# Optimization experiments

Hardware: AMD Instinct MI355X
Metric: run time of the kernel (lower is better)

## Reference

```python
import jax, jax.numpy as jnp
import numpy as np

D_MODEL, N_HEADS, D_HEAD, D_MLP = 768, 12, 64, 3072
B, S = 2, 2048
EPS = 1e-5
IGNORE = -100000.0
INIT = 0.02


def gelu_new(x):
    # GPT-2 'new' gelu: 0.5*x*(1+tanh(sqrt(2/pi)*(x+0.044715*x^3)))
    c = np.sqrt(2.0 / np.pi).astype(np.float32)
    return 0.5 * x * (1.0 + jnp.tanh(c * (x + 0.044715 * x ** 3)))


def layernorm(x, w, b):
    mean = jnp.mean(x, axis=-1, keepdims=True)
    var = jnp.var(x, axis=-1, keepdims=True)
    return (x - mean) / jnp.sqrt(var + EPS) * w + b


def setup_inputs() -> dict:
    key = jax.random.key(0)
    ks = jax.random.split(key, 8)
    return {
        "resid_pre": jax.random.normal(ks[0], (B, S, D_MODEL), dtype=jnp.float32),
        "W_Q": INIT * jax.random.normal(ks[1], (N_HEADS, D_MODEL, D_HEAD), dtype=jnp.float32),
        "b_Q": jnp.zeros((N_HEADS, D_HEAD), jnp.float32),
        "W_K": INIT * jax.random.normal(ks[2], (N_HEADS, D_MODEL, D_HEAD), dtype=jnp.float32),
        "b_K": jnp.zeros((N_HEADS, D_HEAD), jnp.float32),
        "W_V": INIT * jax.random.normal(ks[3], (N_HEADS, D_MODEL, D_HEAD), dtype=jnp.float32),
        "b_V": jnp.zeros((N_HEADS, D_HEAD), jnp.float32),
        "W_O": INIT * jax.random.normal(ks[4], (N_HEADS, D_HEAD, D_MODEL), dtype=jnp.float32),
        "b_O": jnp.zeros((D_MODEL,), jnp.float32),
        "ln1_w": jnp.ones((D_MODEL,), jnp.float32),
        "ln1_b": jnp.zeros((D_MODEL,), jnp.float32),
        "ln2_w": jnp.ones((D_MODEL,), jnp.float32),
        "ln2_b": jnp.zeros((D_MODEL,), jnp.float32),
        "W_in": INIT * jax.random.normal(ks[5], (D_MODEL, D_MLP), dtype=jnp.float32),
        "b_in": jnp.zeros((D_MLP,), jnp.float32),
        "W_out": INIT * jax.random.normal(ks[6], (D_MLP, D_MODEL), dtype=jnp.float32),
        "b_out": jnp.zeros((D_MODEL,), jnp.float32),
    }


def attention(x, W_Q, b_Q, W_K, b_K, W_V, b_V, W_O, b_O):
    # x: [b, s, e]
    q = jnp.einsum('bse,neh->bsnh', x, W_Q) + b_Q
    k = jnp.einsum('bse,neh->bsnh', x, W_K) + b_K
    v = jnp.einsum('bse,neh->bsnh', x, W_V) + b_V
    scores = jnp.einsum('bknh,bqnh->bnqk', k, q) / np.float32(np.sqrt(D_HEAD))
    s = x.shape[1]
    mask = jnp.tril(jnp.ones((s, s), jnp.float32))  # [sq, sk]
    scores = mask * scores + (1.0 - mask) * IGNORE
    probs = jax.nn.softmax(scores, axis=-1)
    z = jnp.einsum('bnqk,bknh->bqnh', probs, v)
    out = jnp.einsum('bqnh,nhe->bqe', z, W_O) + b_O
    return out


def mlp(x, W_in, b_in, W_out, b_out):
    hidden = jnp.einsum('bse,eh->bsh', x, W_in) + b_in
    return jnp.einsum('bsh,he->bse', gelu_new(hidden), W_out) + b_out


def reference(resid_pre, W_Q, b_Q, W_K, b_K, W_V, b_V, W_O, b_O,
              ln1_w, ln1_b, ln2_w, ln2_b, W_in, b_in, W_out, b_out):
    resid_mid = attention(layernorm(resid_pre, ln1_w, ln1_b),
                          W_Q, b_Q, W_K, b_K, W_V, b_V, W_O, b_O) + resid_pre
    out = mlp(layernorm(resid_mid, ln2_w, ln2_b), W_in, b_in, W_out, b_out) + resid_mid
    return out
```

## Files before the change

kernel.cpp:

```cpp
#include <hip/hip_runtime.h>
#include <math.h>

typedef unsigned short ushort_t;
typedef __attribute__((ext_vector_type(8))) short bf16x8;
typedef __attribute__((ext_vector_type(4))) float f32x4;

#define D_MODEL 768
#define N_HEADS 12
#define D_HEAD  64
#define D_MLP   3072
#define BATCH   2
#define SEQ     2048
#define ROWS    (BATCH * SEQ)
#define LN_EPS  1e-5f
#define QKV_LD  2304

__device__ __forceinline__ ushort_t f2bf(float f) {
    unsigned u = __float_as_uint(f);
    u += 0x7fffu + ((u >> 16) & 1u);
    return (ushort_t)(u >> 16);
}
__device__ __forceinline__ float bf2f(ushort_t u) {
    return __uint_as_float((unsigned)u << 16);
}

#define GLD16(g, l) __builtin_amdgcn_global_load_lds( \
    (const __attribute__((address_space(1))) void*)(g), \
    (__attribute__((address_space(3))) void*)(l), 16, 0, 0)

__global__ __launch_bounds__(256) void ln_kernel(const float* __restrict__ x,
                                                 const float* __restrict__ w,
                                                 const float* __restrict__ b,
                                                 ushort_t* __restrict__ y) {
    int row = blockIdx.x;
    const float* xr = x + (size_t)row * D_MODEL;
    float v[3];
    float s = 0.f, sq = 0.f;
#pragma unroll
    for (int u = 0; u < 3; ++u) {
        v[u] = xr[threadIdx.x + u * 256];
        s += v[u];
        sq += v[u] * v[u];
    }
#pragma unroll
    for (int off = 32; off >= 1; off >>= 1) {
        s  += __shfl_xor(s, off);
        sq += __shfl_xor(sq, off);
    }
    __shared__ float ss[4], ssq[4];
    int wave = threadIdx.x >> 6;
    int lane = threadIdx.x & 63;
    if (lane == 0) { ss[wave] = s; ssq[wave] = sq; }
    __syncthreads();
    s = ss[0] + ss[1] + ss[2] + ss[3];
    sq = ssq[0] + ssq[1] + ssq[2] + ssq[3];
    float mean = s * (1.0f / D_MODEL);
    float var = sq * (1.0f / D_MODEL) - mean * mean;
    float rstd = rsqrtf(var + LN_EPS);
    ushort_t* yr = y + (size_t)row * D_MODEL;
#pragma unroll
    for (int u = 0; u < 3; ++u) {
        int idx = threadIdx.x + u * 256;
        yr[idx] = f2bf((v[u] - mean) * rstd * w[idx] + b[idx]);
    }
}

__device__ __forceinline__ float gelu_new_f(float x) {
    float y2 = -1.5957691216057308f * (x + 0.044715f * x * x * x);
    return x / (1.0f + __expf(y2));
}

__device__ __forceinline__ void do_transpose(const float* __restrict__ in, int in_ld, long in_zs,
                                             ushort_t* __restrict__ out, int out_ld, long out_zs,
                                             int bx, int by, int bz) {
    __shared__ float T[64][65];
    long ib = (long)bz * in_zs;
    long ob = (long)bz * out_zs;
    int r0 = bx * 64;
    int c0 = by * 64;
    int tr = threadIdx.x >> 4;
    int tc4 = (threadIdx.x & 15) * 4;
#pragma unroll
    for (int i = 0; i < 4; ++i) {
        int r = i * 16 + tr;
        float4 v = *reinterpret_cast<const float4*>(in + ib + (long)(r0 + r) * in_ld + c0 + tc4);
        T[r][tc4 + 0] = v.x; T[r][tc4 + 1] = v.y;
        T[r][tc4 + 2] = v.z; T[r][tc4 + 3] = v.w;
    }
    __syncthreads();
#pragma unroll
    for (int i = 0; i < 4; ++i) {
        int oc = i * 16 + tr;
        ushort4 o;
        o.x = f2bf(T[tc4 + 0][oc]);
        o.y = f2bf(T[tc4 + 1][oc]);
        o.z = f2bf(T[tc4 + 2][oc]);
        o.w = f2bf(T[tc4 + 3][oc]);
        *reinterpret_cast<ushort4*>(out + ob + (long)(c0 + oc) * out_ld + r0 + tc4) = o;
    }
}

__global__ __launch_bounds__(256) void prep_kernel(
        const float* __restrict__ WQ, const float* __restrict__ WK,
        const float* __restrict__ WV, const float* __restrict__ WO,
        const float* __restrict__ Win, const float* __restrict__ Wout,
        const float* __restrict__ bQ, const float* __restrict__ bK,
        const float* __restrict__ bV,
        ushort_t* __restrict__ wqkvT, ushort_t* __restrict__ woT,
        ushort_t* __restrict__ winT, ushort_t* __restrict__ woutT,
        float* __restrict__ bias_cat) {
    int id = blockIdx.x;
    if (id < 432) {
        int j = id / 144, r = id % 144;
        const float* src = (j == 0) ? WQ : (j == 1) ? WK : WV;
        do_transpose(src, 64, 49152, wqkvT + j * 589824, 768, 49152, r % 12, 0, r / 12);
    } else if (id < 576) {
        int r = id - 432;
        do_transpose(WO, 768, 0, woT, 768, 0, r % 12, r / 12, 0);
    } else if (id < 1152) {
        int r = id - 576;
        do_transpose(Win, 3072, 0, winT, 768, 0, r % 12, r / 12, 0);
    } else if (id < 1728) {
        int r = id - 1152;
        do_transpose(Wout, 768, 0, woutT, 3072, 0, r % 48, r / 48, 0);
    } else {
        for (int i = threadIdx.x; i < 768; i += 256) {
            bias_cat[i] = bQ[i];
            bias_cat[768 + i] = bK[i];
            bias_cat[1536 + i] = bV[i];
        }
    }
}

template <int MODE>
__global__ __launch_bounds__(256) void mfma_gemm(
        const ushort_t* __restrict__ A, int lda,
        const ushort_t* __restrict__ Bt, int ldb,
        const float* __restrict__ bias,
        const float* __restrict__ resid,
        void* __restrict__ C, int cld, int K) {
    __shared__ char As[16384];
    __shared__ char Bs[16384];
    int tid = threadIdx.x;
    int lane = tid & 63, wv = tid >> 6;
    int wr = wv >> 1, wc = wv & 1;
    int l15 = lane & 15, lhi = lane >> 4;
    int m0 = blockIdx.y * 128, n0 = blockIdx.x * 128;

    f32x4 acc[4][4];
#pragma unroll
    for (int i = 0; i < 4; ++i)
#pragma unroll
        for (int j = 0; j < 4; ++j) acc[i][j] = (f32x4)(0.f);

    int srow[4], scol[4];
#pragma unroll
    for (int i = 0; i < 4; ++i) {
        int p = (i * 256 + tid) << 4;
        srow[i] = p >> 7;
        scol[i] = ((p & 127) ^ ((srow[i] & 7) << 4)) >> 1;
    }
    int lbase = wv << 10;

    for (int k0 = 0; k0 < K; k0 += 64) {
#pragma unroll
        for (int i = 0; i < 4; ++i) {
            const ushort_t* ga = A + (size_t)(m0 + srow[i]) * lda + k0 + scol[i];
            GLD16(ga, As + i * 4096 + lbase);
            const ushort_t* gb = Bt + (size_t)(n0 + srow[i]) * ldb + k0 + scol[i];
            GLD16(gb, Bs + i * 4096 + lbase);
        }
        __syncthreads();

        bf16x8 af[4][2], bfr[4][2];
#pragma unroll
        for (int f = 0; f < 4; ++f)
#pragma unroll
            for (int h = 0; h < 2; ++h) {
                int ar = wr * 64 + f * 16 + l15;
                int ac = h * 64 + lhi * 16;
                af[f][h] = *reinterpret_cast<const bf16x8*>(As + ar * 128 + (ac ^ ((ar & 7) << 4)));
                int br = wc * 64 + f * 16 + l15;
                bfr[f][h] = *reinterpret_cast<const bf16x8*>(Bs + br * 128 + (ac ^ ((br & 7) << 4)));
            }
#pragma unroll
        for (int fm = 0; fm < 4; ++fm)
#pragma unroll
            for (int fn = 0; fn < 4; ++fn) {
                acc[fm][fn] = __builtin_amdgcn_mfma_f32_16x16x32_bf16(af[fm][0], bfr[fn][0], acc[fm][fn], 0, 0, 0);
                acc[fm][fn] = __builtin_amdgcn_mfma_f32_16x16x32_bf16(af[fm][1], bfr[fn][1], acc[fm][fn], 0, 0, 0);
            }
        __syncthreads();
    }

#pragma unroll
    for (int fm = 0; fm < 4; ++fm)
#pragma unroll
        for (int fn = 0; fn < 4; ++fn)
#pragma unroll
            for (int i = 0; i < 4; ++i) {
                int m = m0 + wr * 64 + fm * 16 + lhi * 4 + i;
                int n = n0 + wc * 64 + fn * 16 + l15;
                float v = acc[fm][fn][i];
                if (MODE != 3) v += bias[n];
                if (MODE == 0) {
                    ((ushort_t*)C)[(size_t)m * cld + n] = f2bf(v);
                } else if (MODE == 1) {
                    ((float*)C)[(size_t)m * cld + n] = v + resid[(size_t)m * cld + n];
                } else if (MODE == 2) {
                    ((ushort_t*)C)[(size_t)m * cld + n] = f2bf(gelu_new_f(v));
                } else {
                    ((float*)C)[(size_t)m * cld + n] += v;
                }
            }
}

__global__ __launch_bounds__(256) void attn_mfma(ushort_t* __restrict__ qkv) {
    __shared__ char Ks[8192];
    __shared__ char VT[8192];
    __shared__ char Ps[8192];

    int tid = threadIdx.x;
    int lane = tid & 63, wq = tid >> 6;
    int l15 = lane & 15, lhi = lane >> 4;
    int head = blockIdx.y, batch = blockIdx.z;
    size_t rowb = (size_t)batch * SEQ;
    int hcol = head * 64;

    int srow[2], scol[2];
#pragma unroll
    for (int i = 0; i < 2; ++i) {
        int p = (i * 256 + tid) << 4;
        srow[i] = p >> 7;
        scol[i] = ((p & 127) ^ ((srow[i] & 7) << 4)) >> 1;
    }
    char* myPs = Ps + wq * 2048;

    for (int hh = 0; hh < 2; ++hh) {
        int qt = hh ? (int)blockIdx.x : (31 - (int)blockIdx.x);
        int qbase = qt << 6;
        int qb0 = qbase + wq * 16;

        bf16x8 qf[2];
        {
            const ushort_t* qp = qkv + (rowb + qb0 + l15) * QKV_LD + hcol;
            qf[0] = *reinterpret_cast<const bf16x8*>(qp + lhi * 8);
            qf[1] = *reinterpret_cast<const bf16x8*>(qp + 32 + lhi * 8);
        }

        float mrow[4], lrow[4];
        f32x4 o[4];
#pragma unroll
        for (int i = 0; i < 4; ++i) { mrow[i] = -1e30f; lrow[i] = 0.f; o[i] = (f32x4)(0.f); }

        for (int t = 0; t <= qt; ++t) {
            int kt = t << 6;
            __syncthreads();
#pragma unroll
            for (int i = 0; i < 2; ++i) {
                const ushort_t* gk = qkv + (rowb + kt + srow[i]) * QKV_LD + hcol + 768 + scol[i];
                GLD16(gk, Ks + i * 4096 + (wq << 10));
            }
            {
                const ushort_t* vp = qkv + (rowb + kt + lane) * QKV_LD + hcol + 1536 + wq * 16;
#pragma unroll
                for (int u = 0; u < 2; ++u) {
                    uint4 vv = *reinterpret_cast<const uint4*>(vp + u * 8);
                    int d0 = wq * 16 + u * 8;
                    unsigned arr[4] = {vv.x, vv.y, vv.z, vv.w};
#pragma unroll
                    for (int e2 = 0; e2 < 4; ++e2) {
                        int e = e2 * 2;
                        *(ushort_t*)(VT + (d0 + e) * 128 + ((lane << 1) ^ (e << 4))) =
                            (ushort_t)(arr[e2] & 0xffff);
                        *(ushort_t*)(VT + (d0 + e + 1) * 128 + ((lane << 1) ^ ((e + 1) << 4))) =
                            (ushort_t)(arr[e2] >> 16);
                    }
                }
            }
            __syncthreads();

            f32x4 s[4];
#pragma unroll
            for (int f = 0; f < 4; ++f) s[f] = (f32x4)(0.f);
#pragma unroll
            for (int h = 0; h < 2; ++h)
#pragma unroll
                for (int f = 0; f < 4; ++f) {
                    int kr = f * 16 + l15;
                    bf16x8 kf = *reinterpret_cast<const bf16x8*>(
                        Ks + kr * 128 + ((h * 64 + lhi * 16) ^ ((kr & 7) << 4)));
                    s[f] = __builtin_amdgcn_mfma_f32_16x16x32_bf16(qf[h], kf, s[f], 0, 0, 0);
                }

            bool lastT = (t == qt);
#pragma unroll
            for (int i = 0; i < 4; ++i) {
                int q = qb0 + lhi * 4 + i;
                float sv[4];
#pragma unroll
                for (int f = 0; f < 4; ++f) {
                    float x = s[f][i] * 0.125f;
                    if (lastT && (kt + f * 16 + l15 > q)) x = -1e30f;
                    sv[f] = x;
                }
                float tm = fmaxf(fmaxf(sv[0], sv[1]), fmaxf(sv[2], sv[3]));
#pragma unroll
                for (int ofs = 1; ofs <= 8; ofs <<= 1) tm = fmaxf(tm, __shfl_xor(tm, ofs));
                float mn = fmaxf(mrow[i], tm);
                float corr = __expf(mrow[i] - mn);
                mrow[i] = mn;
                float p0 = __expf(sv[0] - mn), p1 = __expf(sv[1] - mn);
                float p2 = __expf(sv[2] - mn), p3 = __expf(sv[3] - mn);
                float su = p0 + p1 + p2 + p3;
#pragma unroll
                for (int ofs = 1; ofs <= 8; ofs <<= 1) su += __shfl_xor(su, ofs);
                lrow[i] = lrow[i] * corr + su;
#pragma unroll
                for (int fn = 0; fn < 4; ++fn) o[fn][i] *= corr;
                int prow = lhi * 4 + i;
                char* pr = myPs + prow * 128;
                int sw = (prow & 7) << 4;
                *(ushort_t*)(pr + (((0 * 16 + l15) << 1) ^ sw)) = f2bf(p0);
                *(ushort_t*)(pr + (((1 * 16 + l15) << 1) ^ sw)) = f2bf(p1);
                *(ushort_t*)(pr + (((2 * 16 + l15) << 1) ^ sw)) = f2bf(p2);
                *(ushort_t*)(pr + (((3 * 16 + l15) << 1) ^ sw)) = f2bf(p3);
            }

#pragma unroll
            for (int h = 0; h < 2; ++h) {
                bf16x8 pa = *reinterpret_cast<const bf16x8*>(
                    myPs + l15 * 128 + ((h * 64 + lhi * 16) ^ ((l15 & 7) << 4)));
#pragma unroll
                for (int fn = 0; fn < 4; ++fn) {
                    int dr = fn * 16 + l15;
                    bf16x8 vf = *reinterpret_cast<const bf16x8*>(
                        VT + dr * 128 + ((h * 64 + lhi * 16) ^ ((dr & 7) << 4)));
                    o[fn] = __builtin_amdgcn_mfma_f32_16x16x32_bf16(pa, vf, o[fn], 0, 0, 0);
                }
            }
        }

#pragma unroll
        for (int i = 0; i < 4; ++i) {
            float inv = 1.0f / lrow[i];
            size_t zr = (rowb + qb0 + lhi * 4 + i) * QKV_LD + hcol;
#pragma unroll
            for (int fn = 0; fn < 4; ++fn)
                qkv[zr + fn * 16 + l15] = f2bf(o[fn][i] * inv);
        }
    }
}

extern "C" void kernel_launch(void* const* d_in, const int* in_sizes, int n_in,
                              void* d_out, int out_size, void* d_ws, size_t ws_size,
                              hipStream_t stream) {
    const float* resid_pre = (const float*)d_in[0];
    const float* W_Q  = (const float*)d_in[1];
    const float* b_Q  = (const float*)d_in[2];
    const float* W_K  = (const float*)d_in[3];
    const float* b_K  = (const float*)d_in[4];
    const float* W_V  = (const float*)d_in[5];
    const float* b_V  = (const float*)d_in[6];
    const float* W_O  = (const float*)d_in[7];
    const float* b_O  = (const float*)d_in[8];
    const float* ln1_w = (const float*)d_in[9];
    const float* ln1_b = (const float*)d_in[10];
    const float* ln2_w = (const float*)d_in[11];
    const float* ln2_b = (const float*)d_in[12];
    const float* W_in  = (const float*)d_in[13];
    const float* b_in  = (const float*)d_in[14];
    const float* W_out = (const float*)d_in[15];
    const float* b_out = (const float*)d_in[16];
    float* out = (float*)d_out;

    ushort_t* ws = (ushort_t*)d_ws;
    ushort_t* qkv    = ws;
    ushort_t* winT   = ws + 9437184;
    ushort_t* woutT  = ws + 11796480;
    ushort_t* wqkvT  = ws + 14155776;
    ushort_t* woT    = ws + 15925248;
    float*    bias_cat = (float*)(ws + 16515072);
    ushort_t* x_ln1  = (ushort_t*)d_out;
    ushort_t* x_ln2  = ws;
    ushort_t* hidden = ws + 3145728;
    float*    resid_mid = out;

    dim3 blk(256);

    prep_kernel<<<1729, blk, 0, stream>>>(W_Q, W_K, W_V, W_O, W_in, W_out,
                                          b_Q, b_K, b_V,
                                          wqkvT, woT, winT, woutT, bias_cat);
    ln_kernel<<<ROWS, blk, 0, stream>>>(resid_pre, ln1_w, ln1_b, x_ln1);
    mfma_gemm<0><<<dim3(18, 32), blk, 0, stream>>>(x_ln1, D_MODEL, wqkvT, D_MODEL,
                                                   bias_cat, nullptr, qkv, QKV_LD, D_MODEL);
    attn_mfma<<<dim3(16, N_HEADS, BATCH), blk, 0, stream>>>(qkv);
    mfma_gemm<1><<<dim3(6, 32), blk, 0, stream>>>(qkv, QKV_LD, woT, D_MODEL,
                                                  b_O, resid_pre, resid_mid, D_MODEL, D_MODEL);
    ln_kernel<<<ROWS, blk, 0, stream>>>(resid_mid, ln2_w, ln2_b, x_ln2);
    for (int b = 0; b < 2; ++b) {
        mfma_gemm<2><<<dim3(12, 32), blk, 0, stream>>>(x_ln2, D_MODEL, winT + b * 1536 * 768, D_MODEL,
                                                       b_in + b * 1536, nullptr, hidden, 1536, D_MODEL);
        if (b == 0) {
            mfma_gemm<1><<<dim3(6, 32), blk, 0, stream>>>(hidden, 1536, woutT + b * 1536, D_MLP,
                                                          b_out, out, out, D_MODEL, 1536);
        } else {
            mfma_gemm<3><<<dim3(6, 32), blk, 0, stream>>>(hidden, 1536, woutT + b * 1536, D_MLP,
                                                          nullptr, nullptr, out, D_MODEL, 1536);
        }
    }
}
```

Measured before the change: 373.2 us.

## Shrink GEMM M-tiles to 64 and split attention into 32-row query tiles

Templates the MFMA GEMM on the M tile size and launches the O-projection and MLP GEMMs with 64-row tiles, doubling their block count so more CUs are filled. The attention kernel moves to 128-thread blocks, each handling 32 query rows per tile with 64 query tiles paired front and back for causal load balance. The goal is better occupancy and wave balance on the many-CU GPU. In exchange, each block reuses its B tile over fewer rows and loads more K/V data per query row.

```diff
diff --git a/kernel.cpp b/kernel.cpp
--- a/kernel.cpp
+++ b/kernel.cpp
@@ -132,24 +132,26 @@
     }
 }
 
-template <int MODE>
+template <int MODE, int TM>
 __global__ __launch_bounds__(256) void mfma_gemm(
         const ushort_t* __restrict__ A, int lda,
         const ushort_t* __restrict__ Bt, int ldb,
         const float* __restrict__ bias,
         const float* __restrict__ resid,
         void* __restrict__ C, int cld, int K) {
-    __shared__ char As[16384];
+    constexpr int FM = TM / 32;
+    constexpr int AISS = TM / 32;
+    __shared__ char As[TM * 128];
     __shared__ char Bs[16384];
     int tid = threadIdx.x;
     int lane = tid & 63, wv = tid >> 6;
     int wr = wv >> 1, wc = wv & 1;
     int l15 = lane & 15, lhi = lane >> 4;
-    int m0 = blockIdx.y * 128, n0 = blockIdx.x * 128;
-
-    f32x4 acc[4][4];
-#pragma unroll
-    for (int i = 0; i < 4; ++i)
+    int m0 = blockIdx.y * TM, n0 = blockIdx.x * 128;
+
+    f32x4 acc[FM][4];
+#pragma unroll
+    for (int i = 0; i < FM; ++i)
 #pragma unroll
         for (int j = 0; j < 4; ++j) acc[i][j] = (f32x4)(0.f);
 
@@ -164,27 +166,36 @@
 
     for (int k0 = 0; k0 < K; k0 += 64) {
 #pragma unroll
-        for (int i = 0; i < 4; ++i) {
+        for (int i = 0; i < AISS; ++i) {
             const ushort_t* ga = A + (size_t)(m0 + srow[i]) * lda + k0 + scol[i];
             GLD16(ga, As + i * 4096 + lbase);
+        }
+#pragma unroll
+        for (int i = 0; i < 4; ++i) {
             const ushort_t* gb = Bt + (size_t)(n0 + srow[i]) * ldb + k0 + scol[i];
             GLD16(gb, Bs + i * 4096 + lbase);
         }
         __syncthreads();
 
-        bf16x8 af[4][2], bfr[4][2];
-#pragma unroll
-        for (int f = 0; f < 4; ++f)
+        bf16x8 af[FM][2], bfr[4][2];
+#pragma unroll
+        for (int f = 0; f < FM; ++f)
 #pragma unroll
             for (int h = 0; h < 2; ++h) {
-                int ar = wr * 64 + f * 16 + l15;
+                int ar = wr * (TM / 2) + f * 16 + l15;
                 int ac = h * 64 + lhi * 16;
                 af[f][h] = *reinterpret_cast<const bf16x8*>(As + ar * 128 + (ac ^ ((ar & 7) << 4)));
+            }
+#pragma unroll
+        for (int f = 0; f < 4; ++f)
+#pragma unroll
+            for (int h = 0; h < 2; ++h) {
                 int br = wc * 64 + f * 16 + l15;
+                int ac = h * 64 + lhi * 16;
                 bfr[f][h] = *reinterpret_cast<const bf16x8*>(Bs + br * 128 + (ac ^ ((br & 7) << 4)));
             }
 #pragma unroll
-        for (int fm = 0; fm < 4; ++fm)
+        for (int fm = 0; fm < FM; ++fm)
 #pragma unroll
             for (int fn = 0; fn < 4; ++fn) {
                 acc[fm][fn] = __builtin_amdgcn_mfma_f32_16x16x32_bf16(af[fm][0], bfr[fn][0], acc[fm][fn], 0, 0, 0);
@@ -194,12 +205,12 @@
     }
 
 #pragma unroll
-    for (int fm = 0; fm < 4; ++fm)
+    for (int fm = 0; fm < FM; ++fm)
 #pragma unroll
         for (int fn = 0; fn < 4; ++fn)
 #pragma unroll
             for (int i = 0; i < 4; ++i) {
-                int m = m0 + wr * 64 + fm * 16 + lhi * 4 + i;
+                int m = m0 + wr * (TM / 2) + fm * 16 + lhi * 4 + i;
                 int n = n0 + wc * 64 + fn * 16 + l15;
                 float v = acc[fm][fn][i];
                 if (MODE != 3) v += bias[n];
@@ -215,10 +226,10 @@
             }
 }
 
-__global__ __launch_bounds__(256) void attn_mfma(ushort_t* __restrict__ qkv) {
+__global__ __launch_bounds__(128) void attn_mfma(ushort_t* __restrict__ qkv) {
     __shared__ char Ks[8192];
     __shared__ char VT[8192];
-    __shared__ char Ps[8192];
+    __shared__ char Ps[4096];
 
     int tid = threadIdx.x;
     int lane = tid & 63, wq = tid >> 6;
@@ -227,19 +238,18 @@
     size_t rowb = (size_t)batch * SEQ;
     int hcol = head * 64;
 
-    int srow[2], scol[2];
-#pragma unroll
-    for (int i = 0; i < 2; ++i) {
-        int p = (i * 256 + tid) << 4;
+    int srow[4], scol[4];
+#pragma unroll
+    for (int i = 0; i < 4; ++i) {
+        int p = (i * 128 + tid) << 4;
         srow[i] = p >> 7;
         scol[i] = ((p & 127) ^ ((srow[i] & 7) << 4)) >> 1;
     }
     char* myPs = Ps + wq * 2048;
 
     for (int hh = 0; hh < 2; ++hh) {
-        int qt = hh ? (int)blockIdx.x : (31 - (int)blockIdx.x);
-        int qbase = qt << 6;
-        int qb0 = qbase + wq * 16;
+        int qt = hh ? (int)blockIdx.x : (63 - (int)blockIdx.x);
+        int qb0 = qt * 32 + wq * 16;
 
         bf16x8 qf[2];
         {
@@ -253,20 +263,21 @@
 #pragma unroll
         for (int i = 0; i < 4; ++i) { mrow[i] = -1e30f; lrow[i] = 0.f; o[i] = (f32x4)(0.f); }
 
-        for (int t = 0; t <= qt; ++t) {
+        int ntiles = qt >> 1;
+        for (int t = 0; t <= ntiles; ++t) {
             int kt = t << 6;
             __syncthreads();
 #pragma unroll
-            for (int i = 0; i < 2; ++i) {
+            for (int i = 0; i < 4; ++i) {
                 const ushort_t* gk = qkv + (rowb + kt + srow[i]) * QKV_LD + hcol + 768 + scol[i];
-                GLD16(gk, Ks + i * 4096 + (wq << 10));
+                GLD16(gk, Ks + i * 2048 + (wq << 10));
             }
             {
-                const ushort_t* vp = qkv + (rowb + kt + lane) * QKV_LD + hcol + 1536 + wq * 16;
-#pragma unroll
-                for (int u = 0; u < 2; ++u) {
+                const ushort_t* vp = qkv + (rowb + kt + lane) * QKV_LD + hcol + 1536 + wq * 32;
+#pragma unroll
+                for (int u = 0; u < 4; ++u) {
                     uint4 vv = *reinterpret_cast<const uint4*>(vp + u * 8);
-                    int d0 = wq * 16 + u * 8;
+                    int d0 = wq * 32 + u * 8;
                     unsigned arr[4] = {vv.x, vv.y, vv.z, vv.w};
 #pragma unroll
                     for (int e2 = 0; e2 < 4; ++e2) {
@@ -293,7 +304,7 @@
                     s[f] = __builtin_amdgcn_mfma_f32_16x16x32_bf16(qf[h], kf, s[f], 0, 0, 0);
                 }
 
-            bool lastT = (t == qt);
+            bool lastT = (t == ntiles);
 #pragma unroll
             for (int i = 0; i < 4; ++i) {
                 int q = qb0 + lhi * 4 + i;
@@ -392,21 +403,21 @@
                                           b_Q, b_K, b_V,
                                           wqkvT, woT, winT, woutT, bias_cat);
     ln_kernel<<<ROWS, blk, 0, stream>>>(resid_pre, ln1_w, ln1_b, x_ln1);
-    mfma_gemm<0><<<dim3(18, 32), blk, 0, stream>>>(x_ln1, D_MODEL, wqkvT, D_MODEL,
-                                                   bias_cat, nullptr, qkv, QKV_LD, D_MODEL);
-    attn_mfma<<<dim3(16, N_HEADS, BATCH), blk, 0, stream>>>(qkv);
-    mfma_gemm<1><<<dim3(6, 32), blk, 0, stream>>>(qkv, QKV_LD, woT, D_MODEL,
-                                                  b_O, resid_pre, resid_mid, D_MODEL, D_MODEL);
+    mfma_gemm<0, 128><<<dim3(18, 32), blk, 0, stream>>>(x_ln1, D_MODEL, wqkvT, D_MODEL,
+                                                        bias_cat, nullptr, qkv, QKV_LD, D_MODEL);
+    attn_mfma<<<dim3(32, N_HEADS, BATCH), dim3(128), 0, stream>>>(qkv);
+    mfma_gemm<1, 64><<<dim3(6, 64), blk, 0, stream>>>(qkv, QKV_LD, woT, D_MODEL,
+                                                      b_O, resid_pre, resid_mid, D_MODEL, D_MODEL);
     ln_kernel<<<ROWS, blk, 0, stream>>>(resid_mid, ln2_w, ln2_b, x_ln2);
     for (int b = 0; b < 2; ++b) {
-        mfma_gemm<2><<<dim3(12, 32), blk, 0, stream>>>(x_ln2, D_MODEL, winT + b * 1536 * 768, D_MODEL,
-                                                       b_in + b * 1536, nullptr, hidden, 1536, D_MODEL);
+        mfma_gemm<2, 64><<<dim3(12, 64), blk, 0, stream>>>(x_ln2, D_MODEL, winT + b * 1536 * 768, D_MODEL,
+                                                           b_in + b * 1536, nullptr, hidden, 1536, D_MODEL);
         if (b == 0) {
-            mfma_gemm<1><<<dim3(6, 32), blk, 0, stream>>>(hidden, 1536, woutT + b * 1536, D_MLP,
-                                                          b_out, out, out, D_MODEL, 1536);
+            mfma_gemm<1, 64><<<dim3(6, 64), blk, 0, stream>>>(hidden, 1536, woutT + b * 1536, D_MLP,
+                                                              b_out, out, out, D_MODEL, 1536);
         } else {
-            mfma_gemm<3><<<dim3(6, 32), blk, 0, stream>>>(hidden, 1536, woutT + b * 1536, D_MLP,
-                                                          nullptr, nullptr, out, D_MODEL, 1536);
-        }
-    }
-}
+            mfma_gemm<3, 64><<<dim3(6, 64), blk, 0, stream>>>(hidden, 1536, woutT + b * 1536, D_MLP,
+                                                              nullptr, nullptr, out, D_MODEL, 1536);
+        }
+    }
+}
```

New measurement: 340.0 us. 8.9% less time.
